# Optimization experiments

Hardware: AMD Instinct MI355X
Metric: run time of the kernel (lower is better)

## Reference

```python
import jax, jax.numpy as jnp
import numpy as np

N_NODES = 10000
N_EDGES = 320000
IN_DIM, HID_DIM, OUT_DIM = 256, 512, 256


def gcn_conv(x, src, dst, W, b, n_nodes):
    """PyG GCNConv: add self-loops, symmetric deg normalization, linear, scatter-add, bias."""
    loops = jnp.arange(n_nodes, dtype=src.dtype)
    s = jnp.concatenate([src, loops])
    d = jnp.concatenate([dst, loops])
    deg = jax.ops.segment_sum(jnp.ones_like(s, dtype=x.dtype), d, num_segments=n_nodes)
    dinv = jax.lax.rsqrt(deg)  # deg >= 1 due to self-loops
    norm = dinv[s] * dinv[d]  # [E+N]
    h = x @ W  # [N, out]
    msg = h[s] * norm[:, None]  # [E+N, out]
    return jax.ops.segment_sum(msg, d, num_segments=n_nodes) + b


def setup_inputs() -> dict:
    key = jax.random.key(0)
    ks = jax.random.split(key, 8)
    x = jax.random.normal(ks[0], (N_NODES, IN_DIM), dtype=jnp.float32)
    edge_index = jax.random.randint(ks[1], (2, N_EDGES), 0, N_NODES, dtype=jnp.int64 if jax.config.jax_enable_x64 else jnp.int32)
    perturb_first = jax.random.normal(ks[2], (N_NODES, HID_DIM), dtype=jnp.float32)
    perturb_last = jax.random.normal(ks[3], (N_NODES, OUT_DIM), dtype=jnp.float32)
    W1 = jax.random.normal(ks[4], (IN_DIM, HID_DIM), dtype=jnp.float32) * (1.0 / np.sqrt(IN_DIM))
    b1 = jnp.zeros((HID_DIM,), dtype=jnp.float32)
    W2 = jax.random.normal(ks[5], (HID_DIM, OUT_DIM), dtype=jnp.float32) * (1.0 / np.sqrt(HID_DIM))
    b2 = jnp.zeros((OUT_DIM,), dtype=jnp.float32)
    return {"x": x, "edge_index": edge_index, "perturb_first": perturb_first,
            "perturb_last": perturb_last, "W1": W1, "b1": b1, "W2": W2, "b2": b2}


def reference(x, edge_index, perturb_first, perturb_last, W1, b1, W2, b2):
    # Faithful to Encoder_Adversarial_GCN.forward: only model[0] (conv1) and
    # model[3] (conv2) are applied; LayerNorm/PReLU layers are skipped.
    src, dst = edge_index[0], edge_index[1]
    h = gcn_conv(x, src, dst, W1, b1, N_NODES) + perturb_first
    out = gcn_conv(h, src, dst, W2, b2, N_NODES) + perturb_last
    return out
```

## Files before the change

### kernel.cpp

```cpp
#include <hip/hip_runtime.h>
#include <hip/hip_bf16.h>

#define NN 10000
#define NE 320000
#define IN_DIM 256
#define HID_DIM 512
#define OUT_DIM 256
#define CAP 96

typedef __attribute__((ext_vector_type(8))) short sh8;
typedef __attribute__((ext_vector_type(4))) float f32x4;

__device__ __forceinline__ ushort f2b(float f) {
    uint u = __builtin_bit_cast(uint, f);
    u = (u + 0x7FFFu + ((u >> 16) & 1u)) >> 16;
    return (ushort)u;
}
__device__ __forceinline__ float b2f(ushort h) {
    uint u = ((uint)h) << 16;
    return __builtin_bit_cast(float, u);
}

__device__ __forceinline__ void g2l16(const ushort* g, ushort* l) {
    __builtin_amdgcn_global_load_lds(
        (const __attribute__((address_space(1))) void*)g,
        (__attribute__((address_space(3))) void*)l,
        16, 0, 0);
}

__global__ void k_conv(const float* __restrict__ x, ushort* __restrict__ xb,
                       const float* __restrict__ W1, ushort* __restrict__ W1t,
                       const float* __restrict__ W2, ushort* __restrict__ W2t,
                       int* __restrict__ cursor) {
    const int b = blockIdx.x, t = threadIdx.x;
    if (b < 2500) {
        size_t i = ((size_t)b * 256 + t) * 4;
        float4 f = *(const float4*)&x[i];
        *(ushort4*)&xb[i] = make_ushort4(f2b(f.x), f2b(f.y), f2b(f.z), f2b(f.w));
    } else if (b < 3012) {
        int idx = (b - 2500) * 256 + t;
        int n = idx >> 8, k = idx & 255;
        W1t[idx] = f2b(W1[(size_t)k * HID_DIM + n]);
    } else if (b < 3524) {
        int idx = (b - 3012) * 256 + t;
        int n = idx >> 9, k = idx & 511;
        W2t[idx] = f2b(W2[(size_t)k * OUT_DIM + n]);
    } else {
        int idx = (b - 3524) * 256 + t;
        cursor[idx] = 0;
    }
}

__global__ void k_fill(const int* __restrict__ src, const int* __restrict__ dst,
                       int* cursor, int* __restrict__ edges, int e) {
    int i = blockIdx.x * blockDim.x + threadIdx.x;
    if (i < e) {
        int d = dst[i];
        int pos = atomicAdd(&cursor[d], 1);
        if (pos < CAP) edges[(size_t)d * CAP + pos] = src[i];
    }
}

template <bool FINAL>
__global__ __launch_bounds__(256) void k_agg(const ushort* __restrict__ tbl,
                                             const int* __restrict__ cnt,
                                             const int* __restrict__ edges,
                                             const float* __restrict__ bias,
                                             const float* __restrict__ pert,
                                             void* __restrict__ outv) {
    const int t = threadIdx.x;
    const int v = blockIdx.x * 4 + (t >> 6);
    const int lane = t & 63;
    const int half = lane >> 5;
    const int d0 = (lane & 31) * 8;
    const int deg = min(cnt[v], CAP);
    const float dv = rsqrtf((float)(deg + 1));
    const int m0 = (deg + 1) >> 1;
    const int* ep = edges + (size_t)v * CAP + (half ? m0 : 0);
    const int n = half ? (deg - m0) : m0;

    float a[8];
    if (half == 0) {
        sh8 hv = *(const sh8*)&tbl[(size_t)v * 256 + d0];
#pragma unroll
        for (int j = 0; j < 8; ++j) a[j] = b2f((ushort)hv[j]) * dv;
    } else {
#pragma unroll
        for (int j = 0; j < 8; ++j) a[j] = 0.f;
    }

    int i = 0;
    for (; i + 4 <= n; i += 4) {
        int s0 = ep[i], s1 = ep[i + 1], s2 = ep[i + 2], s3 = ep[i + 3];
        float w0 = rsqrtf((float)(cnt[s0] + 1));
        float w1 = rsqrtf((float)(cnt[s1] + 1));
        float w2 = rsqrtf((float)(cnt[s2] + 1));
        float w3 = rsqrtf((float)(cnt[s3] + 1));
        sh8 r0 = *(const sh8*)&tbl[(size_t)s0 * 256 + d0];
        sh8 r1 = *(const sh8*)&tbl[(size_t)s1 * 256 + d0];
        sh8 r2 = *(const sh8*)&tbl[(size_t)s2 * 256 + d0];
        sh8 r3 = *(const sh8*)&tbl[(size_t)s3 * 256 + d0];
#pragma unroll
        for (int j = 0; j < 8; ++j) a[j] = fmaf(b2f((ushort)r0[j]), w0, a[j]);
#pragma unroll
        for (int j = 0; j < 8; ++j) a[j] = fmaf(b2f((ushort)r1[j]), w1, a[j]);
#pragma unroll
        for (int j = 0; j < 8; ++j) a[j] = fmaf(b2f((ushort)r2[j]), w2, a[j]);
#pragma unroll
        for (int j = 0; j < 8; ++j) a[j] = fmaf(b2f((ushort)r3[j]), w3, a[j]);
    }
    for (; i < n; ++i) {
        int s0 = ep[i];
        float w0 = rsqrtf((float)(cnt[s0] + 1));
        sh8 r0 = *(const sh8*)&tbl[(size_t)s0 * 256 + d0];
#pragma unroll
        for (int j = 0; j < 8; ++j) a[j] = fmaf(b2f((ushort)r0[j]), w0, a[j]);
    }

#pragma unroll
    for (int j = 0; j < 8; ++j) a[j] = (a[j] + __shfl_xor(a[j], 32)) * dv;

    const int jb = half * 4;
    const size_t o = (size_t)v * 256 + d0 + jb;
    if (FINAL) {
        float* out = (float*)outv;
        float4 pv = *(const float4*)&pert[o];
        float4 bv = *(const float4*)&bias[d0 + jb];
        *(float4*)&out[o] = make_float4(a[jb + 0] + bv.x + pv.x, a[jb + 1] + bv.y + pv.y,
                                        a[jb + 2] + bv.z + pv.z, a[jb + 3] + bv.w + pv.w);
    } else {
        ushort* out = (ushort*)outv;
        *(ushort4*)&out[o] = make_ushort4(f2b(a[jb + 0]), f2b(a[jb + 1]),
                                          f2b(a[jb + 2]), f2b(a[jb + 3]));
    }
}

template <bool BIAS>
__global__ __launch_bounds__(256) void k_gemm(const ushort* __restrict__ A,
                                              const ushort* __restrict__ Bt,
                                              const float* __restrict__ bias,
                                              const float* __restrict__ pert,
                                              ushort* __restrict__ C,
                                              int M, int N, int K) {
    __shared__ ushort As[64][64];
    __shared__ ushort Bs[64][64];
    const int T = gridDim.x;
    const int q = T >> 3, r = T & 7;
    const int xcd = blockIdx.x & 7, jj = blockIdx.x >> 3;
    const int tid = (xcd < r ? xcd * (q + 1) : r * (q + 1) + (xcd - r) * q) + jj;
    const int nbx = N >> 6;
    const int bm = (tid / nbx) * 64;
    const int bn = (tid % nbx) * 64;

    const int t = threadIdx.x;
    const int lane = t & 63;
    const int w = t >> 6;
    const int wm = (w >> 1) * 32, wn = (w & 1) * 32;
    const int fr = lane & 15, kb = lane >> 4;

    const int rho  = lane >> 3;
    const int scol = ((lane & 7) ^ rho) * 8;
    const int c0 = w, c1 = w + 4;
    ushort* lA0 = &As[0][0] + c0 * 512;
    ushort* lA1 = &As[0][0] + c1 * 512;
    ushort* lB0 = &Bs[0][0] + c0 * 512;
    ushort* lB1 = &Bs[0][0] + c1 * 512;
    const ushort* gA0 = A  + (size_t)(bm + c0 * 8 + rho) * K + scol;
    const ushort* gA1 = A  + (size_t)(bm + c1 * 8 + rho) * K + scol;
    const ushort* gB0 = Bt + (size_t)(bn + c0 * 8 + rho) * K + scol;
    const ushort* gB1 = Bt + (size_t)(bn + c1 * 8 + rho) * K + scol;

    f32x4 acc[2][2] = {};

    for (int k0 = 0; k0 < K; k0 += 64) {
        __syncthreads();
        g2l16(gA0, lA0); g2l16(gA1, lA1);
        g2l16(gB0, lB0); g2l16(gB1, lB1);
        gA0 += 64; gA1 += 64; gB0 += 64; gB1 += 64;
        __syncthreads();
#pragma unroll
        for (int ks = 0; ks < 2; ++ks) {
            const int slot = ((ks * 4 + kb) ^ (fr & 7)) * 8;
            sh8 a0 = *(const sh8*)&As[wm + fr][slot];
            sh8 a1 = *(const sh8*)&As[wm + 16 + fr][slot];
            sh8 b0 = *(const sh8*)&Bs[wn + fr][slot];
            sh8 b1 = *(const sh8*)&Bs[wn + 16 + fr][slot];
            acc[0][0] = __builtin_amdgcn_mfma_f32_16x16x32_bf16(a0, b0, acc[0][0], 0, 0, 0);
            acc[0][1] = __builtin_amdgcn_mfma_f32_16x16x32_bf16(a0, b1, acc[0][1], 0, 0, 0);
            acc[1][0] = __builtin_amdgcn_mfma_f32_16x16x32_bf16(a1, b0, acc[1][0], 0, 0, 0);
            acc[1][1] = __builtin_amdgcn_mfma_f32_16x16x32_bf16(a1, b1, acc[1][1], 0, 0, 0);
        }
    }

#pragma unroll
    for (int fm = 0; fm < 2; ++fm)
#pragma unroll
        for (int i = 0; i < 4; ++i) {
            int row = bm + wm + fm * 16 + (lane >> 4) * 4 + i;
            if (row < M) {
#pragma unroll
                for (int fn = 0; fn < 2; ++fn) {
                    int col = bn + wn + fn * 16 + fr;
                    float val = acc[fm][fn][i];
                    if (BIAS) val += bias[col] + pert[(size_t)row * N + col];
                    C[(size_t)row * N + col] = f2b(val);
                }
            }
        }
}

extern "C" void kernel_launch(void* const* d_in, const int* in_sizes, int n_in,
                              void* d_out, int out_size, void* d_ws, size_t ws_size,
                              hipStream_t stream) {
    const float* x  = (const float*)d_in[0];
    const int*   ei = (const int*)d_in[1];
    const float* pf = (const float*)d_in[2];
    const float* pl = (const float*)d_in[3];
    const float* W1 = (const float*)d_in[4];
    const float* b1 = (const float*)d_in[5];
    const float* W2 = (const float*)d_in[6];
    const float* b2 = (const float*)d_in[7];
    float* out = (float*)d_out;

    const int* src = ei;
    const int* dst = ei + NE;

    char* p = (char*)d_ws;
    int*    cursor = (int*)p;            p += 10240 * 4;
    int*    edges  = (int*)p;            p += (size_t)NN * CAP * 4;
    ushort* xb     = (ushort*)p;         p += (size_t)NN * IN_DIM * 2;
    ushort* xa     = (ushort*)p;         p += (size_t)NN * IN_DIM * 2;
    ushort* W1t    = (ushort*)p;         p += (size_t)IN_DIM * HID_DIM * 2;
    ushort* W2t    = (ushort*)p;         p += (size_t)HID_DIM * OUT_DIM * 2;
    ushort* hmid   = (ushort*)p;         p += (size_t)NN * HID_DIM * 2;
    ushort* h2     = (ushort*)p;         p += (size_t)NN * OUT_DIM * 2;

    k_conv<<<3564, 256, 0, stream>>>(x, xb, W1, W1t, W2, W2t, cursor);
    k_fill<<<(NE + 255) / 256, 256, 0, stream>>>(src, dst, cursor, edges, NE);

    const int nby = (NN + 63) / 64;

    k_agg<false><<<NN / 4, 256, 0, stream>>>(xb, cursor, edges, nullptr, nullptr, xa);
    k_gemm<true><<<(HID_DIM / 64) * nby, 256, 0, stream>>>(
        xa, W1t, b1, pf, hmid, NN, HID_DIM, IN_DIM);

    k_gemm<false><<<(OUT_DIM / 64) * nby, 256, 0, stream>>>(
        hmid, W2t, nullptr, nullptr, h2, NN, OUT_DIM, HID_DIM);
    k_agg<true><<<NN / 4, 256, 0, stream>>>(h2, cursor, edges, b2, pl, (void*)out);
}
```

Before: 88.62 us.

## Split aggregation across feature halves and four-way edge partitions per node

The gather-aggregate kernel now gives each block one half of the 256 feature columns, with blocks interleaved so paired node groups sit on different XCD slots. Each wavefront splits a node's edge list into four quarters instead of two, and the partial sums are combined with two cross-lane shuffles. The grid doubles and the inner unroll drops from 4 to 2. The aim is more memory-level parallelism and occupancy for the latency-bound irregular gather, at the cost of more redundant index and degree loads and an extra shuffle stage.

```diff
diff --git a/kernel.cpp b/kernel.cpp
--- a/kernel.cpp
+++ b/kernel.cpp
@@ -69,18 +69,22 @@
                                              const float* __restrict__ pert,
                                              void* __restrict__ outv) {
     const int t = threadIdx.x;
-    const int v = blockIdx.x * 4 + (t >> 6);
+    const int b = blockIdx.x;
+    const int g = b & 7;
+    const int dimhalf = g >> 2;
+    const int nodeblk = (b >> 3) * 4 + (g & 3);
+    const int v = nodeblk * 4 + (t >> 6);
     const int lane = t & 63;
-    const int half = lane >> 5;
-    const int d0 = (lane & 31) * 8;
+    const int qtr = lane >> 4;
+    const int d0 = dimhalf * 128 + (lane & 15) * 8;
     const int deg = min(cnt[v], CAP);
     const float dv = rsqrtf((float)(deg + 1));
-    const int m0 = (deg + 1) >> 1;
-    const int* ep = edges + (size_t)v * CAP + (half ? m0 : 0);
-    const int n = half ? (deg - m0) : m0;
+    const int base = (deg * qtr) >> 2;
+    const int n = ((deg * (qtr + 1)) >> 2) - base;
+    const int* ep = edges + (size_t)v * CAP + base;
 
     float a[8];
-    if (half == 0) {
+    if (qtr == 0) {
         sh8 hv = *(const sh8*)&tbl[(size_t)v * 256 + d0];
 #pragma unroll
         for (int j = 0; j < 8; ++j) a[j] = b2f((ushort)hv[j]) * dv;
@@ -90,26 +94,18 @@
     }
 
     int i = 0;
-    for (; i + 4 <= n; i += 4) {
-        int s0 = ep[i], s1 = ep[i + 1], s2 = ep[i + 2], s3 = ep[i + 3];
+    for (; i + 2 <= n; i += 2) {
+        int s0 = ep[i], s1 = ep[i + 1];
         float w0 = rsqrtf((float)(cnt[s0] + 1));
         float w1 = rsqrtf((float)(cnt[s1] + 1));
-        float w2 = rsqrtf((float)(cnt[s2] + 1));
-        float w3 = rsqrtf((float)(cnt[s3] + 1));
         sh8 r0 = *(const sh8*)&tbl[(size_t)s0 * 256 + d0];
         sh8 r1 = *(const sh8*)&tbl[(size_t)s1 * 256 + d0];
-        sh8 r2 = *(const sh8*)&tbl[(size_t)s2 * 256 + d0];
-        sh8 r3 = *(const sh8*)&tbl[(size_t)s3 * 256 + d0];
 #pragma unroll
         for (int j = 0; j < 8; ++j) a[j] = fmaf(b2f((ushort)r0[j]), w0, a[j]);
 #pragma unroll
         for (int j = 0; j < 8; ++j) a[j] = fmaf(b2f((ushort)r1[j]), w1, a[j]);
-#pragma unroll
-        for (int j = 0; j < 8; ++j) a[j] = fmaf(b2f((ushort)r2[j]), w2, a[j]);
-#pragma unroll
-        for (int j = 0; j < 8; ++j) a[j] = fmaf(b2f((ushort)r3[j]), w3, a[j]);
-    }
-    for (; i < n; ++i) {
+    }
+    if (i < n) {
         int s0 = ep[i];
         float w0 = rsqrtf((float)(cnt[s0] + 1));
         sh8 r0 = *(const sh8*)&tbl[(size_t)s0 * 256 + d0];
@@ -118,20 +114,29 @@
     }
 
 #pragma unroll
-    for (int j = 0; j < 8; ++j) a[j] = (a[j] + __shfl_xor(a[j], 32)) * dv;
-
-    const int jb = half * 4;
-    const size_t o = (size_t)v * 256 + d0 + jb;
-    if (FINAL) {
-        float* out = (float*)outv;
-        float4 pv = *(const float4*)&pert[o];
-        float4 bv = *(const float4*)&bias[d0 + jb];
-        *(float4*)&out[o] = make_float4(a[jb + 0] + bv.x + pv.x, a[jb + 1] + bv.y + pv.y,
-                                        a[jb + 2] + bv.z + pv.z, a[jb + 3] + bv.w + pv.w);
-    } else {
-        ushort* out = (ushort*)outv;
-        *(ushort4*)&out[o] = make_ushort4(f2b(a[jb + 0]), f2b(a[jb + 1]),
-                                          f2b(a[jb + 2]), f2b(a[jb + 3]));
+    for (int j = 0; j < 8; ++j) {
+        a[j] += __shfl_xor(a[j], 16);
+        a[j] += __shfl_xor(a[j], 32);
+        a[j] *= dv;
+    }
+
+    if (qtr == 0) {
+        const size_t o = (size_t)v * 256 + d0;
+        if (FINAL) {
+            float* out = (float*)outv;
+            float4 p0 = *(const float4*)&pert[o];
+            float4 p1 = *(const float4*)&pert[o + 4];
+            float4 b0 = *(const float4*)&bias[d0];
+            float4 b1 = *(const float4*)&bias[d0 + 4];
+            *(float4*)&out[o]     = make_float4(a[0] + b0.x + p0.x, a[1] + b0.y + p0.y,
+                                                a[2] + b0.z + p0.z, a[3] + b0.w + p0.w);
+            *(float4*)&out[o + 4] = make_float4(a[4] + b1.x + p1.x, a[5] + b1.y + p1.y,
+                                                a[6] + b1.z + p1.z, a[7] + b1.w + p1.w);
+        } else {
+            ushort* out = (ushort*)outv;
+            *(ushort4*)&out[o]     = make_ushort4(f2b(a[0]), f2b(a[1]), f2b(a[2]), f2b(a[3]));
+            *(ushort4*)&out[o + 4] = make_ushort4(f2b(a[4]), f2b(a[5]), f2b(a[6]), f2b(a[7]));
+        }
     }
 }
 
@@ -240,11 +245,11 @@
 
     const int nby = (NN + 63) / 64;
 
-    k_agg<false><<<NN / 4, 256, 0, stream>>>(xb, cursor, edges, nullptr, nullptr, xa);
+    k_agg<false><<<(NN / 4) * 2, 256, 0, stream>>>(xb, cursor, edges, nullptr, nullptr, xa);
     k_gemm<true><<<(HID_DIM / 64) * nby, 256, 0, stream>>>(
         xa, W1t, b1, pf, hmid, NN, HID_DIM, IN_DIM);
 
     k_gemm<false><<<(OUT_DIM / 64) * nby, 256, 0, stream>>>(
         hmid, W2t, nullptr, nullptr, h2, NN, OUT_DIM, HID_DIM);
-    k_agg<true><<<NN / 4, 256, 0, stream>>>(h2, cursor, edges, b2, pl, (void*)out);
-}
+    k_agg<true><<<(NN / 4) * 2, 256, 0, stream>>>(h2, cursor, edges, b2, pl, (void*)out);
+}
```

New measurement: 89.23 us. No clear change (+0.7%).
